# Optimization experiments

Hardware: AMD Instinct MI355X
Metric: run time of the kernel (lower is better)

Reference implementation:

```python
import jax, jax.numpy as jnp
import numpy as np

B, N, DIM, H, DH = 2, 2048, 1024, 16, 64
INNER = H * DH
EPS = 1e-12  # F.normalize eps
MAX_LOG_SCALE = np.log(1.0 / 0.01)  # clamp max for logit_scale


def setup_inputs() -> dict:
    key = jax.random.key(0)
    k1, k2, k3, k4 = jax.random.split(key, 4)
    x = jax.random.normal(k1, (B, N, DIM), dtype=jnp.float32)
    # Linear weights stored as [in, out] (transpose of torch's [out, in])
    w_qkv = jax.random.normal(k2, (DIM, 3 * INNER), dtype=jnp.float32) * (DIM ** -0.5)
    w_out = jax.random.normal(k3, (INNER, DIM), dtype=jnp.float32) * (INNER ** -0.5)
    b_out = jax.random.normal(k4, (DIM,), dtype=jnp.float32) * 0.01
    logit_scale = jnp.full((H, 1, 1), jnp.log(10.0), dtype=jnp.float32)
    return {"x": x, "w_qkv": w_qkv, "w_out": w_out, "b_out": b_out,
            "logit_scale": logit_scale}


def reference(x, w_qkv, w_out, b_out, logit_scale):
    b, n, dim = x.shape
    h = logit_scale.shape[0]
    qkv = x @ w_qkv                              # [b, n, 3*inner]
    q, k, v = jnp.split(qkv, 3, axis=-1)
    split_heads = lambda t: t.reshape(b, n, h, -1).transpose(0, 2, 1, 3)  # b h n d
    q, k, v = split_heads(q), split_heads(k), split_heads(v)
    # L2-normalize q and k (F.normalize semantics: divide by max(norm, eps))
    qn = q / jnp.maximum(jnp.linalg.norm(q, axis=-1, keepdims=True), EPS)
    kn = k / jnp.maximum(jnp.linalg.norm(k, axis=-1, keepdims=True), EPS)
    scale = jnp.exp(jnp.minimum(logit_scale, MAX_LOG_SCALE))  # [h,1,1], per-head temp
    cos_dots = jnp.einsum('bhid,bhjd->bhij', qn, kn) * scale   # [b,h,n,n]
    # NOTE: masking in the source mutates the unused plain-dot `dots` tensor,
    # so the output never depends on the mask -> faithfully omitted.
    attn = jax.nn.softmax(cos_dots, axis=-1)
    out = jnp.einsum('bhij,bhjd->bhid', attn, v)               # [b,h,n,d]
    out = out.transpose(0, 2, 1, 3).reshape(b, n, -1)          # [b,n,inner]
    return out @ w_out + b_out
```

## Files before the change

### kernel.cpp

```cpp
#include <hip/hip_runtime.h>

typedef __attribute__((ext_vector_type(8))) short bf16x8;
typedef __attribute__((ext_vector_type(4))) float f32x4;
typedef __attribute__((ext_vector_type(16))) float f32x16;
typedef unsigned short u16;
typedef unsigned int u32;
typedef __attribute__((ext_vector_type(4))) unsigned int u32x4;

#define DEV static __device__ __forceinline__

DEV u16 f2bf(float f) {
  u32 u = __float_as_uint(f);
  u += 0x7FFFu + ((u >> 16) & 1u);
  return (u16)(u >> 16);
}
DEV float bf2f(u16 h) { return __uint_as_float(((u32)h) << 16); }

DEV void gload16(const void* g, void* l) {
  __builtin_amdgcn_global_load_lds((const __attribute__((address_space(1))) void*)g,
                                   (__attribute__((address_space(3))) void*)l, 16, 0, 0);
}

#define MFMA16(a, b, c) __builtin_amdgcn_mfma_f32_16x16x32_bf16((a), (b), (c), 0, 0, 0)
#define MFMA32(a, b, c) __builtin_amdgcn_mfma_f32_32x32x16_bf16((a), (b), (c), 0, 0, 0)

DEV u32 cvtpk(float lo, float hi) {
  u32 r;
  asm("v_cvt_pk_bf16_f32 %0, %1, %2" : "=v"(r) : "v"(lo), "v"(hi));
  return r;
}
DEV void plswap(u32& a, u32& b) {
  asm volatile("v_permlane32_swap_b32 %0, %1" : "+v"(a), "+v"(b));
}
DEV bf16x8 asbf(u32x4 v) {
  union { u32x4 u; bf16x8 b; } x;
  x.u = v;
  return x.b;
}

DEV void rawbar() {
  __builtin_amdgcn_sched_barrier(0);
  asm volatile("" ::: "memory");
  __builtin_amdgcn_s_barrier();
  asm volatile("" ::: "memory");
  __builtin_amdgcn_sched_barrier(0);
}
#define VMCNT4() asm volatile("s_waitcnt vmcnt(4)" ::: "memory")
#define VMCNT0() asm volatile("s_waitcnt vmcnt(0)" ::: "memory")

#define MAXLOG 4.6051701859880914f

__global__ __launch_bounds__(256) void k_prep(const float* __restrict__ x,
                                              u16* __restrict__ Xbf,
                                              const float* __restrict__ w_qkv,
                                              u16* __restrict__ Wqkvt,
                                              const float* __restrict__ w_out,
                                              u16* __restrict__ Woutt) {
  __shared__ u16 lds[64][72];
  int blk = blockIdx.x;
  int t = threadIdx.x;
  if (blk < 2048) {
    int i = blk * 256 + t;
    const f32x4* p = (const f32x4*)(x + (size_t)i * 8);
    f32x4 a = p[0], b = p[1];
    bf16x8 o;
    o[0] = (short)f2bf(a[0]); o[1] = (short)f2bf(a[1]);
    o[2] = (short)f2bf(a[2]); o[3] = (short)f2bf(a[3]);
    o[4] = (short)f2bf(b[0]); o[5] = (short)f2bf(b[1]);
    o[6] = (short)f2bf(b[2]); o[7] = (short)f2bf(b[3]);
    *(bf16x8*)(Xbf + (size_t)i * 8) = o;
    return;
  }
  const float* src;
  u16* dst;
  int rows, cols, bx, by;
  if (blk < 2816) {
    int q = blk - 2048;
    src = w_qkv; dst = Wqkvt; rows = 1024; cols = 3072;
    bx = q % 48; by = q / 48;
  } else {
    int q = blk - 2816;
    src = w_out; dst = Woutt; rows = 1024; cols = 1024;
    bx = q % 16; by = q / 16;
  }
  int r0 = by * 64, c0 = bx * 64;
  int r = t >> 2, cq = (t & 3) << 4;
  const float* s = src + (size_t)(r0 + r) * cols + c0 + cq;
#pragma unroll
  for (int i = 0; i < 16; i += 4) {
    f32x4 v = *(const f32x4*)(s + i);
    lds[r][cq + i + 0] = f2bf(v[0]);
    lds[r][cq + i + 1] = f2bf(v[1]);
    lds[r][cq + i + 2] = f2bf(v[2]);
    lds[r][cq + i + 3] = f2bf(v[3]);
  }
  __syncthreads();
  int c = t >> 2, rq = (t & 3) << 4;
  bf16x8 o0, o1;
#pragma unroll
  for (int i = 0; i < 8; ++i) o0[i] = (short)lds[rq + i][c];
#pragma unroll
  for (int i = 0; i < 8; ++i) o1[i] = (short)lds[rq + 8 + i][c];
  u16* d = dst + (size_t)(c0 + c) * rows + r0 + rq;
  *(bf16x8*)d = o0;
  *(bf16x8*)(d + 8) = o1;
}

template <bool OUT_BF16, bool HAS_BIAS>
__global__ __launch_bounds__(256) void k_gemm_bt(const u16* __restrict__ A,
                                                 const u16* __restrict__ Bt,
                                                 void* __restrict__ Cout,
                                                 const float* __restrict__ bias,
                                                 int M, int N, int K, int nbx) {
  __shared__ __align__(16) u16 lsA[128 * 32];
  __shared__ __align__(16) u16 lsB[128 * 32];
  int tid = threadIdx.x;
  int lane = tid & 63, wave = tid >> 6;
  int wr = (wave >> 1) * 64, wc = (wave & 1) * 64;
  int nwg = gridDim.x;
  int orig = blockIdx.x;
  int wg = (orig & 7) * (nwg >> 3) + (orig >> 3);
  int bm = (wg / nbx) * 128, bn = (wg % nbx) * 128;

  f32x4 acc[4][4] = {};

  const u16* aSrc[2]; u16* aDst[2];
  const u16* bSrc[2]; u16* bDst[2];
#pragma unroll
  for (int j = 0; j < 2; ++j) {
    int s = wave * 128 + j * 64 + lane;
    int row = s >> 2, chunk = s & 3;
    int g = chunk ^ ((row >> 1) & 3);
    aSrc[j] = A + (size_t)(bm + row) * K + g * 8;
    bSrc[j] = Bt + (size_t)(bn + row) * K + g * 8;
    aDst[j] = &lsA[(wave * 128 + j * 64) * 8];
    bDst[j] = &lsB[(wave * 128 + j * 64) * 8];
  }

  for (int k0 = 0; k0 < K; k0 += 32) {
    __syncthreads();
    gload16(aSrc[0] + k0, aDst[0]);
    gload16(aSrc[1] + k0, aDst[1]);
    gload16(bSrc[0] + k0, bDst[0]);
    gload16(bSrc[1] + k0, bDst[1]);
    __syncthreads();
    bf16x8 af[4], bfr[4];
#pragma unroll
    for (int m = 0; m < 4; ++m) {
      int r = wr + m * 16 + (lane & 15);
      int p = (lane >> 4) ^ ((r >> 1) & 3);
      af[m] = *(const bf16x8*)&lsA[r * 32 + p * 8];
    }
#pragma unroll
    for (int n = 0; n < 4; ++n) {
      int r = wc + n * 16 + (lane & 15);
      int p = (lane >> 4) ^ ((r >> 1) & 3);
      bfr[n] = *(const bf16x8*)&lsB[r * 32 + p * 8];
    }
#pragma unroll
    for (int m = 0; m < 4; ++m)
#pragma unroll
      for (int n = 0; n < 4; ++n)
        acc[m][n] = MFMA16(af[m], bfr[n], acc[m][n]);
  }

#pragma unroll
  for (int m = 0; m < 4; ++m) {
    int row = bm + wr + m * 16 + ((lane >> 4) << 2);
#pragma unroll
    for (int n = 0; n < 4; ++n) {
      int col = bn + wc + n * 16 + (lane & 15);
#pragma unroll
      for (int j = 0; j < 4; ++j) {
        if (OUT_BF16) {
          ((u16*)Cout)[(size_t)(row + j) * N + col] = f2bf(acc[m][n][j]);
        } else {
          float bb = HAS_BIAS ? bias[col] : 0.f;
          ((float*)Cout)[(size_t)(row + j) * N + col] = acc[m][n][j] + bb;
        }
      }
    }
  }
}

__global__ __launch_bounds__(256) void k_gemm_out(const u16* __restrict__ A,
                                                  const u16* __restrict__ Bt,
                                                  float* __restrict__ Cout,
                                                  const float* __restrict__ bias,
                                                  int M, int N, int K, int nbx) {
  __shared__ __align__(16) u16 lsA[128 * 32];
  __shared__ __align__(16) u16 lsB[64 * 32];
  int tid = threadIdx.x;
  int lane = tid & 63, wave = tid >> 6;
  int wr = (wave >> 1) * 64, wc = (wave & 1) * 32;
  int nwg = gridDim.x;
  int orig = blockIdx.x;
  int wg = (orig & 7) * (nwg >> 3) + (orig >> 3);
  int bm = (wg / nbx) * 128, bn = (wg % nbx) * 64;

  f32x4 acc[4][2] = {};

  const u16* aSrc[2]; u16* aDst[2];
  const u16* bSrc;    u16* bDst;
#pragma unroll
  for (int j = 0; j < 2; ++j) {
    int s = wave * 128 + j * 64 + lane;
    int row = s >> 2, chunk = s & 3;
    int g = chunk ^ ((row >> 1) & 3);
    aSrc[j] = A + (size_t)(bm + row) * K + g * 8;
    aDst[j] = &lsA[(wave * 128 + j * 64) * 8];
  }
  {
    int s = wave * 64 + lane;
    int row = s >> 2, chunk = s & 3;
    int g = chunk ^ ((row >> 1) & 3);
    bSrc = Bt + (size_t)(bn + row) * K + g * 8;
    bDst = &lsB[(wave * 64) * 8];
  }

  for (int k0 = 0; k0 < K; k0 += 32) {
    __syncthreads();
    gload16(aSrc[0] + k0, aDst[0]);
    gload16(aSrc[1] + k0, aDst[1]);
    gload16(bSrc + k0, bDst);
    __syncthreads();
    bf16x8 af[4], bfr[2];
#pragma unroll
    for (int m = 0; m < 4; ++m) {
      int r = wr + m * 16 + (lane & 15);
      int p = (lane >> 4) ^ ((r >> 1) & 3);
      af[m] = *(const bf16x8*)&lsA[r * 32 + p * 8];
    }
#pragma unroll
    for (int n = 0; n < 2; ++n) {
      int r = wc + n * 16 + (lane & 15);
      int p = (lane >> 4) ^ ((r >> 1) & 3);
      bfr[n] = *(const bf16x8*)&lsB[r * 32 + p * 8];
    }
#pragma unroll
    for (int m = 0; m < 4; ++m)
#pragma unroll
      for (int n = 0; n < 2; ++n)
        acc[m][n] = MFMA16(af[m], bfr[n], acc[m][n]);
  }

#pragma unroll
  for (int m = 0; m < 4; ++m) {
    int row = bm + wr + m * 16 + ((lane >> 4) << 2);
#pragma unroll
    for (int n = 0; n < 2; ++n) {
      int col = bn + wc + n * 16 + (lane & 15);
      float bb = bias[col];
#pragma unroll
      for (int j = 0; j < 4; ++j)
        Cout[(size_t)(row + j) * N + col] = acc[m][n][j] + bb;
    }
  }
}

__global__ __launch_bounds__(256) void k_qkpack(const u16* __restrict__ QKV,
                                                const float* __restrict__ logit_scale,
                                                u16* __restrict__ Qn, u16* __restrict__ Kn,
                                                u16* __restrict__ Vt) {
  __shared__ u16 lds[64][72];
  int blk = blockIdx.x;
  int tid = threadIdx.x;
  if (blk < 256) {
    int idx = blk * 256 + tid;
    int n = idx & 2047, bh = idx >> 11;
    int b = bh >> 4, h = bh & 15;
    float scale = __expf(fminf(logit_scale[h], MAXLOG));
    const u16* qp = QKV + ((size_t)(b * 2048 + n)) * 3072 + h * 64;
    bf16x8 qv[8], kv[8];
#pragma unroll
    for (int j = 0; j < 8; ++j) {
      qv[j] = *(const bf16x8*)(qp + j * 8);
      kv[j] = *(const bf16x8*)(qp + 1024 + j * 8);
    }
    float sq = 0.f, sk = 0.f;
#pragma unroll
    for (int j = 0; j < 8; ++j)
#pragma unroll
      for (int e = 0; e < 8; ++e) {
        float fq = bf2f((u16)qv[j][e]);
        float fk = bf2f((u16)kv[j][e]);
        sq += fq * fq;
        sk += fk * fk;
      }
    float rq = scale / fmaxf(sqrtf(sq), 1e-12f);
    float rk = 1.0f / fmaxf(sqrtf(sk), 1e-12f);
    u16* qo = Qn + ((size_t)bh * 2048 + n) * 64;
    u16* ko = Kn + ((size_t)bh * 2048 + n) * 64;
#pragma unroll
    for (int j = 0; j < 8; ++j) {
      bf16x8 oq, ok;
#pragma unroll
      for (int e = 0; e < 8; ++e) {
        oq[e] = (short)f2bf(bf2f((u16)qv[j][e]) * rq);
        ok[e] = (short)f2bf(bf2f((u16)kv[j][e]) * rk);
      }
      *(bf16x8*)(qo + j * 8) = oq;
      *(bf16x8*)(ko + j * 8) = ok;
    }
    return;
  }
  int q = blk - 256;
  int nt = q & 31, h = (q >> 5) & 15, b = q >> 9;
  int bh = b * 16 + h;
  int r = tid >> 2, cq = (tid & 3) << 4;
  size_t voff = ((size_t)(b * 2048 + nt * 64 + r)) * 3072 + 2048 + h * 64 + cq;
  *(bf16x8*)&lds[r][cq] = *(const bf16x8*)&QKV[voff];
  *(bf16x8*)&lds[r][cq + 8] = *(const bf16x8*)&QKV[voff + 8];
  __syncthreads();
  int d = tid >> 2, nq = (tid & 3) << 4;
  bf16x8 o0, o1;
#pragma unroll
  for (int i = 0; i < 8; ++i) o0[i] = (short)lds[nq + i][d];
#pragma unroll
  for (int i = 0; i < 8; ++i) o1[i] = (short)lds[nq + 8 + i][d];
  u16* vd = Vt + ((size_t)bh * 64 + d) * 2048 + nt * 64 + nq;
  *(bf16x8*)vd = o0;
  *(bf16x8*)(vd + 8) = o1;
}

__global__ __launch_bounds__(256, 2) void k_flash(const u16* __restrict__ Qn,
                                                  const u16* __restrict__ Kn,
                                                  const u16* __restrict__ Vt,
                                                  const float* __restrict__ logit_scale,
                                                  u16* __restrict__ AO) {
  __shared__ __align__(16) u16 lsK[2][64 * 64];
  __shared__ __align__(16) u16 lsV[2][64 * 64];
  __shared__ float l_s[4][32];
  int tid = threadIdx.x, lane = tid & 63, wave = tid >> 6;
  int r31 = lane & 31, h = lane >> 5;
  int bh = blockIdx.x, b = bh >> 4, hd = bh & 15;
  int qw = blockIdx.y * 128 + wave * 32;
  const u16* Q = Qn + (size_t)bh * 2048 * 64;
  const u16* Kb = Kn + (size_t)bh * 2048 * 64;
  const u16* Vb = Vt + (size_t)bh * 64 * 2048;

  float negC = -__expf(fminf(logit_scale[hd], MAXLOG));

  bf16x8 qB[4];
#pragma unroll
  for (int ks = 0; ks < 4; ++ks)
    qB[ks] = *(const bf16x8*)&Q[(size_t)(qw + r31) * 64 + ks * 16 + h * 8];

  size_t kGO[2], vGO[2];
  int lOff[2];
#pragma unroll
  for (int j = 0; j < 2; ++j) {
    int s = j * 256 + tid;
    int row = s >> 3, ch = s & 7, g = ch ^ (row & 7);
    kGO[j] = (size_t)row * 64 + g * 8;
    vGO[j] = (size_t)row * 2048 + g * 8;
    lOff[j] = s * 8;
  }

  int off[2][4];
#pragma unroll
  for (int a = 0; a < 2; ++a)
#pragma unroll
    for (int ks = 0; ks < 4; ++ks)
      off[a][ks] = (a * 32 + r31) * 64 + ((((ks << 1) | h) ^ (r31 & 7)) << 3);

  f32x16 o0, o1;
#pragma unroll
  for (int i = 0; i < 16; ++i) { o0[i] = 0.f; o1[i] = 0.f; }
  float lsum = 0.f;

#define STAGE(dstbuf, kvt)                                          \
  {                                                                 \
    size_t kv0 = (size_t)(kvt) * 64;                                \
    gload16(Kb + kv0 * 64 + kGO[0], &lsK[dstbuf][lOff[0]]);         \
    gload16(Kb + kv0 * 64 + kGO[1], &lsK[dstbuf][lOff[1]]);         \
    gload16(Vb + kv0 + vGO[0], &lsV[dstbuf][lOff[0]]);              \
    gload16(Vb + kv0 + vGO[1], &lsV[dstbuf][lOff[1]]);              \
  }

  STAGE(0, 0);

#pragma unroll 1
  for (int t = 0; t < 32; ++t) {
    int cur = t & 1;
    if (t < 31) {
      STAGE(cur ^ 1, t + 1);
      VMCNT4();
    } else {
      VMCNT0();
    }
    rawbar();
    const u16* Kl = lsK[cur];
    const u16* Vl = lsV[cur];

    f32x16 s0, s1;
#pragma unroll
    for (int i = 0; i < 16; ++i) { s0[i] = negC; s1[i] = negC; }
    bf16x8 k0f[4], k1f[4];
#pragma unroll
    for (int ks = 0; ks < 4; ++ks) {
      k0f[ks] = *(const bf16x8*)&Kl[off[0][ks]];
      k1f[ks] = *(const bf16x8*)&Kl[off[1][ks]];
    }
    __builtin_amdgcn_s_setprio(1);
#pragma unroll
    for (int ks = 0; ks < 4; ++ks) {
      s0 = MFMA32(k0f[ks], qB[ks], s0);
      s1 = MFMA32(k1f[ks], qB[ks], s1);
    }
    __builtin_amdgcn_s_setprio(0);

    bf16x8 v0f[4], v1f[4];
#pragma unroll
    for (int ks = 0; ks < 4; ++ks) {
      v0f[ks] = *(const bf16x8*)&Vl[off[0][ks]];
      v1f[ks] = *(const bf16x8*)&Vl[off[1][ks]];
    }

#pragma unroll
    for (int i = 0; i < 16; ++i) {
      float e0 = __expf(s0[i]);
      float e1 = __expf(s1[i]);
      lsum += e0 + e1;
      s0[i] = e0; s1[i] = e1;
    }

    bf16x8 pa[4];
    {
      u32 c0 = cvtpk(s0[0], s0[1]),  c1 = cvtpk(s0[2], s0[3]);
      u32 c2 = cvtpk(s0[4], s0[5]),  c3 = cvtpk(s0[6], s0[7]);
      u32 c4 = cvtpk(s0[8], s0[9]),  c5 = cvtpk(s0[10], s0[11]);
      u32 c6 = cvtpk(s0[12], s0[13]), c7 = cvtpk(s0[14], s0[15]);
      plswap(c0, c2); plswap(c1, c3); plswap(c4, c6); plswap(c5, c7);
      pa[0] = asbf((u32x4){c0, c1, c2, c3});
      pa[1] = asbf((u32x4){c4, c5, c6, c7});
      u32 d0 = cvtpk(s1[0], s1[1]),  d1 = cvtpk(s1[2], s1[3]);
      u32 d2 = cvtpk(s1[4], s1[5]),  d3 = cvtpk(s1[6], s1[7]);
      u32 d4 = cvtpk(s1[8], s1[9]),  d5 = cvtpk(s1[10], s1[11]);
      u32 d6 = cvtpk(s1[12], s1[13]), d7 = cvtpk(s1[14], s1[15]);
      plswap(d0, d2); plswap(d1, d3); plswap(d4, d6); plswap(d5, d7);
      pa[2] = asbf((u32x4){d0, d1, d2, d3});
      pa[3] = asbf((u32x4){d4, d5, d6, d7});
    }

    __builtin_amdgcn_s_setprio(1);
#pragma unroll
    for (int ks = 0; ks < 4; ++ks) {
      o0 = MFMA32(pa[ks], v0f[ks], o0);
      o1 = MFMA32(pa[ks], v1f[ks], o1);
    }
    __builtin_amdgcn_s_setprio(0);

    rawbar();
  }
#undef STAGE

  float ltot = lsum + __shfl_xor(lsum, 32, 64);
  if (h == 0) l_s[wave][r31] = 1.0f / ltot;
  __syncthreads();

#pragma unroll
  for (int r = 0; r < 16; ++r) {
    int cr = (r & 3) + ((r >> 2) << 3) + (h << 2);
    int qr = qw + cr;
    float li = l_s[wave][cr];
    size_t base = ((size_t)(b * 2048 + qr)) * 1024 + hd * 64;
    AO[base + r31] = f2bf(o0[r] * li);
    AO[base + 32 + r31] = f2bf(o1[r] * li);
  }
}

extern "C" void kernel_launch(void* const* d_in, const int* in_sizes, int n_in,
                              void* d_out, int out_size, void* d_ws, size_t ws_size,
                              hipStream_t stream) {
  const float* x = (const float*)d_in[0];
  const float* w_qkv = (const float*)d_in[1];
  const float* w_out = (const float*)d_in[2];
  const float* b_out = (const float*)d_in[3];
  const float* logit_scale = (const float*)d_in[4];

  char* ws = (char*)d_ws;
  u16* Xbf   = (u16*)(ws);
  u16* Wqkvt = (u16*)(ws + (8ll << 20));
  u16* Woutt = (u16*)(ws + (14ll << 20));
  u16* QKV   = (u16*)(ws + (16ll << 20));
  u16* Qn    = (u16*)(ws + (40ll << 20));
  u16* Kn    = (u16*)(ws + (48ll << 20));
  u16* Vt    = (u16*)(ws + (56ll << 20));
  u16* AO    = Xbf;
  float* out = (float*)d_out;

  k_prep<<<3072, 256, 0, stream>>>(x, Xbf, w_qkv, Wqkvt, w_out, Woutt);
  k_gemm_bt<true, false><<<768, 256, 0, stream>>>(Xbf, Wqkvt, QKV, nullptr,
                                                  4096, 3072, 1024, 24);
  k_qkpack<<<1280, 256, 0, stream>>>(QKV, logit_scale, Qn, Kn, Vt);
  k_flash<<<dim3(32, 16), 256, 0, stream>>>(Qn, Kn, Vt, logit_scale, AO);
  k_gemm_out<<<512, 256, 0, stream>>>(AO, Woutt, out, b_out,
                                      4096, 1024, 1024, 16);
}
```

Baseline: 128.7 us.

## Fuse q/k normalization and V transpose into QKV GEMM epilogue

The QKV projection GEMM now writes normalized, temperature-scaled Q and normalized K directly in head-major layout. Row norms are reduced across lanes with shuffles over the 64-column wave tile, which matches one head. V tiles are transposed through LDS in the epilogue and stored as Vt. This removes the separate pack kernel and the bf16 QKV intermediate round trip through global memory. In exchange the epilogue does more work and makes scattered stores; norms are now computed from fp32 accumulators instead of rounded bf16 values.

```diff
diff --git a/kernel.cpp b/kernel.cpp
--- a/kernel.cpp
+++ b/kernel.cpp
@@ -47,6 +47,7 @@
 }
 #define VMCNT4() asm volatile("s_waitcnt vmcnt(4)" ::: "memory")
 #define VMCNT0() asm volatile("s_waitcnt vmcnt(0)" ::: "memory")
+#define LGKM0()  asm volatile("s_waitcnt lgkmcnt(0)" ::: "memory")
 
 #define MAXLOG 4.6051701859880914f
 
@@ -106,12 +107,12 @@
   *(bf16x8*)(d + 8) = o1;
 }
 
-template <bool OUT_BF16, bool HAS_BIAS>
-__global__ __launch_bounds__(256) void k_gemm_bt(const u16* __restrict__ A,
-                                                 const u16* __restrict__ Bt,
-                                                 void* __restrict__ Cout,
-                                                 const float* __restrict__ bias,
-                                                 int M, int N, int K, int nbx) {
+__global__ __launch_bounds__(256) void k_gemm_qkv(const u16* __restrict__ A,
+                                                  const u16* __restrict__ Bt,
+                                                  const float* __restrict__ logit_scale,
+                                                  u16* __restrict__ Qn, u16* __restrict__ Kn,
+                                                  u16* __restrict__ Vt,
+                                                  int M, int N, int K, int nbx) {
   __shared__ __align__(16) u16 lsA[128 * 32];
   __shared__ __align__(16) u16 lsB[128 * 32];
   int tid = threadIdx.x;
@@ -164,21 +165,64 @@
         acc[m][n] = MFMA16(af[m], bfr[n], acc[m][n]);
   }
 
-#pragma unroll
-  for (int m = 0; m < 4; ++m) {
-    int row = bm + wr + m * 16 + ((lane >> 4) << 2);
-#pragma unroll
-    for (int n = 0; n < 4; ++n) {
-      int col = bn + wc + n * 16 + (lane & 15);
+  int colg = bn + wc;
+  if (colg < 2048) {
+    bool isQ = colg < 1024;
+    int h = (colg >> 6) & 15;
+    float scale = isQ ? __expf(fminf(logit_scale[h], MAXLOG)) : 1.0f;
+    u16* dst = isQ ? Qn : Kn;
+#pragma unroll
+    for (int m = 0; m < 4; ++m) {
 #pragma unroll
       for (int j = 0; j < 4; ++j) {
-        if (OUT_BF16) {
-          ((u16*)Cout)[(size_t)(row + j) * N + col] = f2bf(acc[m][n][j]);
-        } else {
-          float bb = HAS_BIAS ? bias[col] : 0.f;
-          ((float*)Cout)[(size_t)(row + j) * N + col] = acc[m][n][j] + bb;
-        }
+        float ss = 0.f;
+#pragma unroll
+        for (int n = 0; n < 4; ++n) ss += acc[m][n][j] * acc[m][n][j];
+        ss += __shfl_xor(ss, 1, 64);
+        ss += __shfl_xor(ss, 2, 64);
+        ss += __shfl_xor(ss, 4, 64);
+        ss += __shfl_xor(ss, 8, 64);
+        float r = scale / fmaxf(sqrtf(ss), 1e-12f);
+        int row = bm + wr + m * 16 + ((lane >> 4) << 2) + j;
+        int b = row >> 11, tok = row & 2047;
+        size_t base = ((size_t)(b * 16 + h) * 2048 + tok) * 64;
+#pragma unroll
+        for (int n = 0; n < 4; ++n)
+          dst[base + n * 16 + (lane & 15)] = f2bf(acc[m][n][j] * r);
       }
+    }
+  } else {
+    int h = ((colg - 2048) >> 6) & 15;
+    __syncthreads();
+    u16* sl = (wave < 2 ? lsA : lsB) + (wave & 1) * 2048;
+    int bb = bm >> 11, bmm = bm & 2047;
+    size_t vbase = ((size_t)(bb * 16 + h) * 64) * 2048;
+#pragma unroll
+    for (int rr = 0; rr < 2; ++rr) {
+#pragma unroll
+      for (int nn = 0; nn < 2; ++nn) {
+        int n = rr * 2 + nn;
+        int d32 = nn * 16 + (lane & 15);
+        int xr = (d32 & 7) << 3;
+#pragma unroll
+        for (int m = 0; m < 4; ++m)
+#pragma unroll
+          for (int j = 0; j < 4; ++j) {
+            int tok = m * 16 + ((lane >> 4) << 2) + j;
+            sl[d32 * 64 + (tok ^ xr)] = f2bf(acc[m][n][j]);
+          }
+      }
+      LGKM0();
+#pragma unroll
+      for (int ri = 0; ri < 4; ++ri) {
+        int li = ri * 64 + lane;
+        int d32 = li >> 3, c = li & 7;
+        int cx = c ^ (d32 & 7);
+        bf16x8 v = *(const bf16x8*)&sl[d32 * 64 + cx * 8];
+        size_t dsto = vbase + (size_t)(rr * 32 + d32) * 2048 + bmm + wr + c * 8;
+        *(bf16x8*)&Vt[dsto] = v;
+      }
+      LGKM0();
     }
   }
 }
@@ -256,71 +300,6 @@
         Cout[(size_t)(row + j) * N + col] = acc[m][n][j] + bb;
     }
   }
-}
-
-__global__ __launch_bounds__(256) void k_qkpack(const u16* __restrict__ QKV,
-                                                const float* __restrict__ logit_scale,
-                                                u16* __restrict__ Qn, u16* __restrict__ Kn,
-                                                u16* __restrict__ Vt) {
-  __shared__ u16 lds[64][72];
-  int blk = blockIdx.x;
-  int tid = threadIdx.x;
-  if (blk < 256) {
-    int idx = blk * 256 + tid;
-    int n = idx & 2047, bh = idx >> 11;
-    int b = bh >> 4, h = bh & 15;
-    float scale = __expf(fminf(logit_scale[h], MAXLOG));
-    const u16* qp = QKV + ((size_t)(b * 2048 + n)) * 3072 + h * 64;
-    bf16x8 qv[8], kv[8];
-#pragma unroll
-    for (int j = 0; j < 8; ++j) {
-      qv[j] = *(const bf16x8*)(qp + j * 8);
-      kv[j] = *(const bf16x8*)(qp + 1024 + j * 8);
-    }
-    float sq = 0.f, sk = 0.f;
-#pragma unroll
-    for (int j = 0; j < 8; ++j)
-#pragma unroll
-      for (int e = 0; e < 8; ++e) {
-        float fq = bf2f((u16)qv[j][e]);
-        float fk = bf2f((u16)kv[j][e]);
-        sq += fq * fq;
-        sk += fk * fk;
-      }
-    float rq = scale / fmaxf(sqrtf(sq), 1e-12f);
-    float rk = 1.0f / fmaxf(sqrtf(sk), 1e-12f);
-    u16* qo = Qn + ((size_t)bh * 2048 + n) * 64;
-    u16* ko = Kn + ((size_t)bh * 2048 + n) * 64;
-#pragma unroll
-    for (int j = 0; j < 8; ++j) {
-      bf16x8 oq, ok;
-#pragma unroll
-      for (int e = 0; e < 8; ++e) {
-        oq[e] = (short)f2bf(bf2f((u16)qv[j][e]) * rq);
-        ok[e] = (short)f2bf(bf2f((u16)kv[j][e]) * rk);
-      }
-      *(bf16x8*)(qo + j * 8) = oq;
-      *(bf16x8*)(ko + j * 8) = ok;
-    }
-    return;
-  }
-  int q = blk - 256;
-  int nt = q & 31, h = (q >> 5) & 15, b = q >> 9;
-  int bh = b * 16 + h;
-  int r = tid >> 2, cq = (tid & 3) << 4;
-  size_t voff = ((size_t)(b * 2048 + nt * 64 + r)) * 3072 + 2048 + h * 64 + cq;
-  *(bf16x8*)&lds[r][cq] = *(const bf16x8*)&QKV[voff];
-  *(bf16x8*)&lds[r][cq + 8] = *(const bf16x8*)&QKV[voff + 8];
-  __syncthreads();
-  int d = tid >> 2, nq = (tid & 3) << 4;
-  bf16x8 o0, o1;
-#pragma unroll
-  for (int i = 0; i < 8; ++i) o0[i] = (short)lds[nq + i][d];
-#pragma unroll
-  for (int i = 0; i < 8; ++i) o1[i] = (short)lds[nq + 8 + i][d];
-  u16* vd = Vt + ((size_t)bh * 64 + d) * 2048 + nt * 64 + nq;
-  *(bf16x8*)vd = o0;
-  *(bf16x8*)(vd + 8) = o1;
 }
 
 __global__ __launch_bounds__(256, 2) void k_flash(const u16* __restrict__ Qn,
@@ -483,17 +462,15 @@
   u16* Xbf   = (u16*)(ws);
   u16* Wqkvt = (u16*)(ws + (8ll << 20));
   u16* Woutt = (u16*)(ws + (14ll << 20));
-  u16* QKV   = (u16*)(ws + (16ll << 20));
-  u16* Qn    = (u16*)(ws + (40ll << 20));
-  u16* Kn    = (u16*)(ws + (48ll << 20));
-  u16* Vt    = (u16*)(ws + (56ll << 20));
+  u16* Qn    = (u16*)(ws + (16ll << 20));
+  u16* Kn    = (u16*)(ws + (24ll << 20));
+  u16* Vt    = (u16*)(ws + (32ll << 20));
   u16* AO    = Xbf;
   float* out = (float*)d_out;
 
   k_prep<<<3072, 256, 0, stream>>>(x, Xbf, w_qkv, Wqkvt, w_out, Woutt);
-  k_gemm_bt<true, false><<<768, 256, 0, stream>>>(Xbf, Wqkvt, QKV, nullptr,
-                                                  4096, 3072, 1024, 24);
-  k_qkpack<<<1280, 256, 0, stream>>>(QKV, logit_scale, Qn, Kn, Vt);
+  k_gemm_qkv<<<768, 256, 0, stream>>>(Xbf, Wqkvt, logit_scale, Qn, Kn, Vt,
+                                      4096, 3072, 1024, 24);
   k_flash<<<dim3(32, 16), 256, 0, stream>>>(Qn, Kn, Vt, logit_scale, AO);
   k_gemm_out<<<512, 256, 0, stream>>>(AO, Woutt, out, b_out,
                                       4096, 1024, 1024, 16);
```

New measurement: 117.7 us. 1.09x faster.
